# Kernel optimization log

Hardware: AMD Instinct MI355X
Metric: run time of the kernel (lower is better)

The kernel has to match this reference:

```python
import jax, jax.numpy as jnp
import numpy as np

B, L, H, V = 2, 1024, 64, 32000
HID = 4 * H  # hidden_dim = num_harmonics * 4


def setup_inputs() -> dict:
    key = jax.random.key(0)
    ks = jax.random.split(key, 12)
    freqs = jax.random.normal(ks[0], (B, L, H), dtype=jnp.float32)
    amps = jax.random.uniform(ks[1], (B, L, H), dtype=jnp.float32)  # positive so log1p(sum) is finite
    phases = jax.random.normal(ks[2], (B, L, H), dtype=jnp.float32)
    wave_repr = jnp.concatenate([freqs, amps, phases], axis=-1)  # [B, L, 3H]
    s = 0.05
    return {
        "wave_repr": wave_repr,
        "vocab_frequencies": jax.random.normal(ks[3], (V, H), dtype=jnp.float32),
        "vocab_phases": jax.random.normal(ks[4], (V, H), dtype=jnp.float32) * 0.5,
        "W0": jax.random.normal(ks[5], (3 * H, HID), dtype=jnp.float32) * s,
        "b0": jnp.zeros((HID,), dtype=jnp.float32),
        "W1": jax.random.normal(ks[6], (HID, HID), dtype=jnp.float32) * s,
        "b1": jnp.zeros((HID,), dtype=jnp.float32),
        "W2": jax.random.normal(ks[7], (HID, HID), dtype=jnp.float32) * s,
        "b2": jnp.zeros((HID,), dtype=jnp.float32),
        "Wv": jax.random.normal(ks[8], (HID, V), dtype=jnp.float32) * s,
        "bv": jnp.zeros((V,), dtype=jnp.float32),
        "residual_weights": jnp.full((3,), 0.5, dtype=jnp.float32),
    }


def _gelu(x):
    return jax.nn.gelu(x, approximate=False)  # torch F.gelu default = exact erf


def reference(wave_repr, vocab_frequencies, vocab_phases, W0, b0, W1, b1, W2, b2, Wv, bv, residual_weights):
    h = vocab_frequencies.shape[1]
    freqs = wave_repr[..., :h]
    amps = wave_repr[..., h:2 * h]
    phases = wave_repr[..., 2 * h:]

    # synthesis MLP: layer 0 has no residual; layers 1..2 add weighted residual
    x = _gelu(wave_repr @ W0 + b0)
    for i, (W, b) in enumerate(((W1, b1), (W2, b2)), start=1):
        res = x
        x = _gelu(x @ W + b) + residual_weights[i] * res

    # freq_similarity = -cdist(freqs, vocab_frequencies): expanded as one GEMM
    f2 = jnp.sum(freqs * freqs, axis=-1, keepdims=True)           # [B,L,1]
    v2 = jnp.sum(vocab_frequencies * vocab_frequencies, axis=-1)  # [V]
    cross = jnp.einsum('blh,vh->blv', freqs, vocab_frequencies)   # [B,L,V]
    freq_similarity = -jnp.sqrt(jnp.maximum(f2 + v2 - 2.0 * cross, 0.0))

    # mean_h cos(phase - vocab_phase) via cos(a-b) = cos a cos b + sin a sin b (two GEMMs)
    phase_coherence = (
        jnp.einsum('blh,vh->blv', jnp.cos(phases), jnp.cos(vocab_phases))
        + jnp.einsum('blh,vh->blv', jnp.sin(phases), jnp.sin(vocab_phases))
    ) / h

    amp_energy = jnp.sum(amps, axis=-1, keepdims=True)  # [B,L,1]
    pattern_match = (freq_similarity + 0.5 * phase_coherence) * jnp.log1p(amp_energy)

    synthesis_proj = x @ Wv + bv  # [B,L,V]
    return pattern_match + 0.1 * synthesis_proj
```

## Files before the change

### kernel.cpp

```cpp
#include <hip/hip_runtime.h>
#include <hip/hip_bf16.h>

typedef unsigned short u16;
typedef __attribute__((ext_vector_type(8))) unsigned short u16x8;
typedef __attribute__((ext_vector_type(8))) short short8;
typedef __attribute__((ext_vector_type(4))) float f32x4;

#define VCOLS 32000
#define ASTRIDE 448
#define BSTRIDE 448

__device__ __forceinline__ u16 f2bf(float f) {
    union { float f; unsigned u; } x; x.f = f;
    unsigned r = x.u + 0x7FFF + ((x.u >> 16) & 1);
    return (u16)(r >> 16);
}

__device__ __forceinline__ float gelu_exact(float v) {
    return 0.5f * v * (1.0f + erff(v * 0.70710678118654752f));
}

__device__ __forceinline__ void gload_lds16(const void* g, void* l) {
    __builtin_amdgcn_global_load_lds(
        (const __attribute__((address_space(1))) unsigned int*)g,
        (__attribute__((address_space(3))) unsigned int*)l, 16, 0, 0);
}

#define RP_ROWS 8
__global__ __launch_bounds__(256) void row_prep(
    const float* __restrict__ wr,
    const float* __restrict__ W0, const float* __restrict__ b0,
    const float* __restrict__ W1, const float* __restrict__ b1,
    const float* __restrict__ W2, const float* __restrict__ b2,
    const float* __restrict__ rw,
    u16* __restrict__ Ag, float* __restrict__ rowstats)
{
    __shared__ float in_s[RP_ROWS * 192];
    __shared__ float x_s[RP_ROWS * 256];
    __shared__ float y_s[RP_ROWS * 256];
    __shared__ u16  row_s[RP_ROWS][448];
    __shared__ float la_s[RP_ROWS];

    const int t = threadIdx.x;
    const int r0 = blockIdx.x * RP_ROWS;

    for (int i = t; i < RP_ROWS * 192; i += 256)
        in_s[i] = wr[(size_t)r0 * 192 + i];
    __syncthreads();

    {
        int row = t >> 5, j = t & 31;
        float a0 = in_s[row*192 + j],      a1 = in_s[row*192 + 32 + j];
        float f2p = a0*a0 + a1*a1;
        float ampp = in_s[row*192 + 64 + j] + in_s[row*192 + 96 + j];
        #pragma unroll
        for (int m = 16; m >= 1; m >>= 1) {
            f2p  += __shfl_xor(f2p, m);
            ampp += __shfl_xor(ampp, m);
        }
        if (j == 0) {
            float la = log1pf(ampp);
            la_s[row] = la;
            rowstats[(size_t)(r0+row)*2]     = f2p;
            rowstats[(size_t)(r0+row)*2 + 1] = la;
        }
    }
    const float rw1 = rw[1], rw2 = rw[2];

    float acc[RP_ROWS], res[RP_ROWS];

    #pragma unroll
    for (int r = 0; r < RP_ROWS; ++r) acc[r] = 0.f;
    for (int k0 = 0; k0 < 192; k0 += 16) {
        float w[16];
        #pragma unroll
        for (int e = 0; e < 16; ++e) w[e] = W0[(k0+e)*256 + t];
        #pragma unroll
        for (int e = 0; e < 16; ++e) {
            #pragma unroll
            for (int r = 0; r < RP_ROWS; ++r) acc[r] += in_s[r*192 + k0 + e] * w[e];
        }
    }
    {
        float bb = b0[t];
        #pragma unroll
        for (int r = 0; r < RP_ROWS; ++r) {
            float v = gelu_exact(acc[r] + bb);
            res[r] = v; x_s[r*256 + t] = v;
        }
    }
    __syncthreads();

    #pragma unroll
    for (int r = 0; r < RP_ROWS; ++r) acc[r] = 0.f;
    for (int k0 = 0; k0 < 256; k0 += 16) {
        float w[16];
        #pragma unroll
        for (int e = 0; e < 16; ++e) w[e] = W1[(k0+e)*256 + t];
        #pragma unroll
        for (int e = 0; e < 16; ++e) {
            #pragma unroll
            for (int r = 0; r < RP_ROWS; ++r) acc[r] += x_s[r*256 + k0 + e] * w[e];
        }
    }
    {
        float bb = b1[t];
        #pragma unroll
        for (int r = 0; r < RP_ROWS; ++r) {
            float v = gelu_exact(acc[r] + bb) + rw1 * res[r];
            res[r] = v; y_s[r*256 + t] = v;
        }
    }
    __syncthreads();

    #pragma unroll
    for (int r = 0; r < RP_ROWS; ++r) acc[r] = 0.f;
    for (int k0 = 0; k0 < 256; k0 += 16) {
        float w[16];
        #pragma unroll
        for (int e = 0; e < 16; ++e) w[e] = W2[(k0+e)*256 + t];
        #pragma unroll
        for (int e = 0; e < 16; ++e) {
            #pragma unroll
            for (int r = 0; r < RP_ROWS; ++r) acc[r] += y_s[r*256 + k0 + e] * w[e];
        }
    }
    {
        float bb = b2[t];
        #pragma unroll
        for (int r = 0; r < RP_ROWS; ++r)
            res[r] = gelu_exact(acc[r] + bb) + rw2 * res[r];
    }

    #pragma unroll
    for (int r = 0; r < RP_ROWS; ++r)
        row_s[r][192 + t] = f2bf(0.1f * res[r]);
    if (t < 64) {
        #pragma unroll
        for (int r = 0; r < RP_ROWS; ++r)
            row_s[r][t] = f2bf(in_s[r*192 + t]);
    } else if (t < 128) {
        int h = t - 64;
        #pragma unroll
        for (int r = 0; r < RP_ROWS; ++r) {
            float s, c; __sincosf(in_s[r*192 + 128 + h], &s, &c);
            row_s[r][t] = f2bf(c * (0.5f/64.f) * la_s[r]);
        }
    } else if (t < 192) {
        int h = t - 128;
        #pragma unroll
        for (int r = 0; r < RP_ROWS; ++r) {
            float s, c; __sincosf(in_s[r*192 + 128 + h], &s, &c);
            row_s[r][t] = f2bf(s * (0.5f/64.f) * la_s[r]);
        }
    }
    __syncthreads();

    for (int idx = t; idx < RP_ROWS * 56; idx += 256) {
        int r = idx / 56, c = idx % 56;
        int kt = c >> 3, ac = c & 7;
        int m = r0 + r;
        u16x8 val = *(const u16x8*)&row_s[r][c*8];
        *(u16x8*)(Ag + (size_t)m*ASTRIDE + kt*64 + ((ac ^ (m & 7)) * 8)) = val;
    }
}

__global__ __launch_bounds__(256) void vocab_prep(
    const float* __restrict__ vf, const float* __restrict__ vp,
    const float* __restrict__ Wv,
    u16* __restrict__ Bg, float* __restrict__ v2)
{
    __shared__ float wv_s[64][68];

    const int t = threadIdx.x;
    const int v0 = blockIdx.x * 64;

    {
        int v = v0 + (t >> 2);
        int q = t & 3;
        int s = v & 7;
        u16x8* baseB = (u16x8*)(Bg + (size_t)v * BSTRIDE);

        const float4* src = (const float4*)(vf + (size_t)v*64 + q*16);
        float ss = 0.f;
        u16 tf[16];
        #pragma unroll
        for (int i = 0; i < 4; ++i) {
            float4 x = src[i];
            ss += x.x*x.x + x.y*x.y + x.z*x.z + x.w*x.w;
            tf[i*4+0] = f2bf(x.x); tf[i*4+1] = f2bf(x.y);
            tf[i*4+2] = f2bf(x.z); tf[i*4+3] = f2bf(x.w);
        }
        u16x8 o0, o1;
        #pragma unroll
        for (int e = 0; e < 8; ++e) { o0[e] = tf[e]; o1[e] = tf[8+e]; }
        baseB[(2*q) ^ s]     = o0;
        baseB[(2*q+1) ^ s]   = o1;

        ss += __shfl_xor(ss, 1);
        ss += __shfl_xor(ss, 2);
        if (q == 0) v2[v] = ss;

        const float4* sp = (const float4*)(vp + (size_t)v*64 + q*16);
        u16 tc[16], ts_[16];
        #pragma unroll
        for (int i = 0; i < 4; ++i) {
            float4 x = sp[i];
            float sn, cs;
            __sincosf(x.x, &sn, &cs); tc[i*4+0] = f2bf(cs); ts_[i*4+0] = f2bf(sn);
            __sincosf(x.y, &sn, &cs); tc[i*4+1] = f2bf(cs); ts_[i*4+1] = f2bf(sn);
            __sincosf(x.z, &sn, &cs); tc[i*4+2] = f2bf(cs); ts_[i*4+2] = f2bf(sn);
            __sincosf(x.w, &sn, &cs); tc[i*4+3] = f2bf(cs); ts_[i*4+3] = f2bf(sn);
        }
        u16x8 c0, c1, s0, s1;
        #pragma unroll
        for (int e = 0; e < 8; ++e) { c0[e]=tc[e]; c1[e]=tc[8+e]; s0[e]=ts_[e]; s1[e]=ts_[8+e]; }
        baseB[8  + ((2*q) ^ s)]   = c0;
        baseB[8  + ((2*q+1) ^ s)] = c1;
        baseB[16 + ((2*q) ^ s)]   = s0;
        baseB[16 + ((2*q+1) ^ s)] = s1;
    }

    for (int kc = 0; kc < 4; ++kc) {
        __syncthreads();
        {
            int r = t >> 2, q = t & 3;
            const float4* src = (const float4*)(Wv + (size_t)(kc*64 + r)*VCOLS + v0 + q*16);
            float4* dst = (float4*)&wv_s[r][q*16];
            dst[0] = src[0]; dst[1] = src[1]; dst[2] = src[2]; dst[3] = src[3];
        }
        __syncthreads();
        {
            int v = t & 63, g = t >> 6;
            int s = (v0 + v) & 7;
            u16x8* baseB = (u16x8*)(Bg + (size_t)(v0 + v) * BSTRIDE);
            #pragma unroll
            for (int cc = 0; cc < 2; ++cc) {
                int ch = g*2 + cc;
                u16x8 o;
                #pragma unroll
                for (int e = 0; e < 8; ++e) o[e] = f2bf(wv_s[ch*8 + e][v]);
                baseB[(3 + kc)*8 + (ch ^ s)] = o;
            }
        }
    }
}

__global__ __launch_bounds__(256, 2) void spectral_main(
    const u16* __restrict__ Ag, const u16* __restrict__ Bg,
    const float* __restrict__ rowstats, const float* __restrict__ v2,
    const float* __restrict__ bv, float* __restrict__ out)
{
    __shared__ u16 As[2][128 * 64];
    __shared__ u16 Bs[2][128 * 64];

    const int bid = blockIdx.x;
    const int l   = (bid & 7) * 500 + (bid >> 3);
    const int tm  = l / 250;
    const int tn  = l % 250;
    const int rowA0 = tm * 128;
    const int colB0 = tn * 128;

    const int tid  = threadIdx.x;
    const int wv   = tid >> 6, lane = tid & 63;
    const int wm   = (wv >> 1) * 64, wn = (wv & 1) * 64;
    const int cg   = lane >> 4, ln = lane & 15;

    f32x4 acc[4][4] = {};

    auto stage = [&](int kt, int buf) {
        const u16* ab = Ag + (size_t)(rowA0 + wv*32 + (lane >> 3)) * ASTRIDE + kt*64 + (lane & 7)*8;
        u16* al = As[buf] + wv*2048 + lane*8;
        #pragma unroll
        for (int c = 0; c < 4; ++c)
            gload_lds16(ab + (size_t)c*8*ASTRIDE, al + c*512);
        const u16* bb = Bg + (size_t)(colB0 + wv*32 + (lane >> 3)) * BSTRIDE + kt*64 + (lane & 7)*8;
        u16* bl = Bs[buf] + wv*2048 + lane*8;
        #pragma unroll
        for (int c = 0; c < 4; ++c)
            gload_lds16(bb + (size_t)c*8*BSTRIDE, bl + c*512);
    };

    auto compute = [&](int buf) {
        #pragma unroll
        for (int kk = 0; kk < 2; ++kk) {
            short8 a[4], b[4];
            #pragma unroll
            for (int fr = 0; fr < 4; ++fr) {
                int r = wm + fr*16 + ln;
                a[fr] = *(const short8*)&As[buf][r*64 + (((kk*4 + cg) ^ (ln & 7)) * 8)];
            }
            #pragma unroll
            for (int fc = 0; fc < 4; ++fc) {
                int r = wn + fc*16 + ln;
                b[fc] = *(const short8*)&Bs[buf][r*64 + (((kk*4 + cg) ^ (ln & 7)) * 8)];
            }
            #pragma unroll
            for (int fr = 0; fr < 4; ++fr)
                #pragma unroll
                for (int fc = 0; fc < 4; ++fc)
                    acc[fr][fc] = __builtin_amdgcn_mfma_f32_16x16x32_bf16(
                        a[fr], b[fc], acc[fr][fc], 0, 0, 0);
        }
    };

    stage(0, 0);
    int cur = 0;
    for (int kt = 0; kt < 7; ++kt) {
        if (kt < 6) {
            stage(kt + 1, cur ^ 1);
            asm volatile("s_waitcnt vmcnt(8)" ::: "memory");
        } else {
            asm volatile("s_waitcnt vmcnt(0)" ::: "memory");
        }
        __builtin_amdgcn_s_barrier();
        compute(cur);

        if (kt == 0) {
            float f2m[4][4], lam[4][4], v2n[4], bvn[4];
            #pragma unroll
            for (int fr = 0; fr < 4; ++fr)
                #pragma unroll
                for (int j = 0; j < 4; ++j) {
                    int m = rowA0 + wm + fr*16 + cg*4 + j;
                    f2m[fr][j] = rowstats[(size_t)2*m];
                    lam[fr][j] = rowstats[(size_t)2*m + 1];
                }
            #pragma unroll
            for (int fc = 0; fc < 4; ++fc) {
                int n = colB0 + wn + fc*16 + ln;
                v2n[fc] = v2[n];
                bvn[fc] = bv[n];
            }
            #pragma unroll
            for (int fr = 0; fr < 4; ++fr)
                #pragma unroll
                for (int fc = 0; fc < 4; ++fc)
                    #pragma unroll
                    for (int j = 0; j < 4; ++j) {
                        float cross = acc[fr][fc][j];
                        float arg = fmaxf(f2m[fr][j] + v2n[fc] - 2.0f*cross, 0.0f);
                        acc[fr][fc][j] = 0.1f*bvn[fc] - lam[fr][j]*sqrtf(arg);
                    }
        }

        asm volatile("" ::: "memory");
        __builtin_amdgcn_s_barrier();
        cur ^= 1;
    }

    #pragma unroll
    for (int fr = 0; fr < 4; ++fr)
        #pragma unroll
        for (int fc = 0; fc < 4; ++fc)
            #pragma unroll
            for (int j = 0; j < 4; ++j) {
                int m = rowA0 + wm + fr*16 + cg*4 + j;
                int n = colB0 + wn + fc*16 + ln;
                out[(size_t)m * VCOLS + n] = acc[fr][fc][j];
            }
}

extern "C" void kernel_launch(void* const* d_in, const int* in_sizes, int n_in,
                              void* d_out, int out_size, void* d_ws, size_t ws_size,
                              hipStream_t stream) {
    const float* wave_repr = (const float*)d_in[0];
    const float* vf  = (const float*)d_in[1];
    const float* vp  = (const float*)d_in[2];
    const float* W0  = (const float*)d_in[3];
    const float* b0  = (const float*)d_in[4];
    const float* W1  = (const float*)d_in[5];
    const float* b1  = (const float*)d_in[6];
    const float* W2  = (const float*)d_in[7];
    const float* b2  = (const float*)d_in[8];
    const float* Wv  = (const float*)d_in[9];
    const float* bv  = (const float*)d_in[10];
    const float* rw  = (const float*)d_in[11];
    float* out = (float*)d_out;

    u16*   Ag       = (u16*)d_ws;
    u16*   Bg       = (u16*)((char*)d_ws + 1835008);
    float* rowstats = (float*)((char*)d_ws + 30507008);
    float* v2       = (float*)((char*)d_ws + 30523392);

    hipLaunchKernelGGL(row_prep, dim3(2048 / RP_ROWS), dim3(256), 0, stream,
                       wave_repr, W0, b0, W1, b1, W2, b2, rw, Ag, rowstats);
    hipLaunchKernelGGL(vocab_prep, dim3(VCOLS / 64), dim3(256), 0, stream,
                       vf, vp, Wv, Bg, v2);
    hipLaunchKernelGGL(spectral_main, dim3(16 * 250), dim3(256), 0, stream,
                       Ag, Bg, rowstats, v2, bv, out);
}
```

Before: 458.6 us.

## Drop LDS double buffering to raise occupancy to three blocks per CU

Replaces the double-buffered A/B shared-memory tiles with single buffers, halving LDS use, and raises the launch-bounds minimum blocks per CU from 2 to 3. The prefetch of the next k-tile is removed; each tile is now loaded after the previous compute and a barrier. The intent is to hide global-load latency through more resident blocks rather than intra-block pipelining. The risk is that loads and MFMA work are serialized within each block and the tighter register budget could cause spills.

New measurement: 446.4 us. -2.7%, faster.

```diff
diff --git a/kernel.cpp b/kernel.cpp
--- a/kernel.cpp
+++ b/kernel.cpp
@@ -246,13 +246,13 @@
     }
 }
 
-__global__ __launch_bounds__(256, 2) void spectral_main(
+__global__ __launch_bounds__(256, 3) void spectral_main(
     const u16* __restrict__ Ag, const u16* __restrict__ Bg,
     const float* __restrict__ rowstats, const float* __restrict__ v2,
     const float* __restrict__ bv, float* __restrict__ out)
 {
-    __shared__ u16 As[2][128 * 64];
-    __shared__ u16 Bs[2][128 * 64];
+    __shared__ u16 As[128 * 64];
+    __shared__ u16 Bs[128 * 64];
 
     const int bid = blockIdx.x;
     const int l   = (bid & 7) * 500 + (bid >> 3);
@@ -268,32 +268,32 @@
 
     f32x4 acc[4][4] = {};
 
-    auto stage = [&](int kt, int buf) {
+    auto stage = [&](int kt) {
         const u16* ab = Ag + (size_t)(rowA0 + wv*32 + (lane >> 3)) * ASTRIDE + kt*64 + (lane & 7)*8;
-        u16* al = As[buf] + wv*2048 + lane*8;
+        u16* al = As + wv*2048 + lane*8;
         #pragma unroll
         for (int c = 0; c < 4; ++c)
             gload_lds16(ab + (size_t)c*8*ASTRIDE, al + c*512);
         const u16* bb = Bg + (size_t)(colB0 + wv*32 + (lane >> 3)) * BSTRIDE + kt*64 + (lane & 7)*8;
-        u16* bl = Bs[buf] + wv*2048 + lane*8;
+        u16* bl = Bs + wv*2048 + lane*8;
         #pragma unroll
         for (int c = 0; c < 4; ++c)
             gload_lds16(bb + (size_t)c*8*BSTRIDE, bl + c*512);
     };
 
-    auto compute = [&](int buf) {
+    auto compute = [&]() {
         #pragma unroll
         for (int kk = 0; kk < 2; ++kk) {
             short8 a[4], b[4];
             #pragma unroll
             for (int fr = 0; fr < 4; ++fr) {
                 int r = wm + fr*16 + ln;
-                a[fr] = *(const short8*)&As[buf][r*64 + (((kk*4 + cg) ^ (ln & 7)) * 8)];
+                a[fr] = *(const short8*)&As[r*64 + (((kk*4 + cg) ^ (ln & 7)) * 8)];
             }
             #pragma unroll
             for (int fc = 0; fc < 4; ++fc) {
                 int r = wn + fc*16 + ln;
-                b[fc] = *(const short8*)&Bs[buf][r*64 + (((kk*4 + cg) ^ (ln & 7)) * 8)];
+                b[fc] = *(const short8*)&Bs[r*64 + (((kk*4 + cg) ^ (ln & 7)) * 8)];
             }
             #pragma unroll
             for (int fr = 0; fr < 4; ++fr)
@@ -304,17 +304,10 @@
         }
     };
 
-    stage(0, 0);
-    int cur = 0;
+    stage(0);
     for (int kt = 0; kt < 7; ++kt) {
-        if (kt < 6) {
-            stage(kt + 1, cur ^ 1);
-            asm volatile("s_waitcnt vmcnt(8)" ::: "memory");
-        } else {
-            asm volatile("s_waitcnt vmcnt(0)" ::: "memory");
-        }
-        __builtin_amdgcn_s_barrier();
-        compute(cur);
+        __syncthreads();
+        compute();
 
         if (kt == 0) {
             float f2m[4][4], lam[4][4], v2n[4], bvn[4];
@@ -344,9 +337,8 @@
                     }
         }
 
-        asm volatile("" ::: "memory");
-        __builtin_amdgcn_s_barrier();
-        cur ^= 1;
+        __syncthreads();
+        if (kt < 6) stage(kt + 1);
     }
 
     #pragma unroll
```
